# Optimization experiments

Measured on AMD Instinct MI355X. Metric: run time of the kernel, lower is better.

## Reference

```python
import jax, jax.numpy as jnp
import numpy as np

T = 2048          # tokens (single-sequence prefill)
HID = 4096        # hidden_size
NH = 32           # num attention heads
NKV = 8           # num kv heads (GQA)
HD = 128          # head_dim
QKV_OUT = (NH + 2 * NKV) * HD  # 6144
THETA = 10000.0
SCALING = HD ** -0.5


def setup_inputs() -> dict:
    key = jax.random.key(0)
    ks = jax.random.split(key, 8)
    positions = jnp.arange(T, dtype=jnp.int32)
    # per-token int8 quantized hidden states (symmetric, [-127,127])
    q_act = jax.random.randint(ks[0], (T, HID), -127, 128, dtype=jnp.int32)
    # per-token dynamic activation scale
    act_scale = jax.random.uniform(ks[1], (T,), jnp.float32) * 0.01 + 0.001
    # int4 weights stored unsigned [0,15] with per-output-channel scale & zero point
    w_qkv_q = jax.random.randint(ks[2], (QKV_OUT, HID), 0, 16, dtype=jnp.int32)
    w_qkv_scale = jax.random.uniform(ks[3], (QKV_OUT,), jnp.float32) * 0.01 + 0.001
    w_qkv_zero = jax.random.uniform(ks[4], (QKV_OUT,), jnp.float32) * 2.0 + 7.0
    w_o_q = jax.random.randint(ks[5], (HID, HID), 0, 16, dtype=jnp.int32)
    w_o_scale = jax.random.uniform(ks[6], (HID,), jnp.float32) * 0.01 + 0.001
    w_o_zero = jax.random.uniform(ks[7], (HID,), jnp.float32) * 2.0 + 7.0
    return dict(positions=positions, q_act=q_act, act_scale=act_scale,
                w_qkv_q=w_qkv_q, w_qkv_scale=w_qkv_scale, w_qkv_zero=w_qkv_zero,
                w_o_q=w_o_q, w_o_scale=w_o_scale, w_o_zero=w_o_zero)


def w4a8_linear(qa_f, s_a, a_sum, qw, s_w, z_w):
    # y[t,o] = s_a[t]*s_w[o] * ( (qa @ qw^T)[t,o] - z_w[o]*sum_j qa[t,j] )
    acc = jnp.matmul(qa_f, qw.astype(jnp.float32).T)  # [T, O]
    return (s_a[:, None] * s_w[None, :]) * (acc - z_w[None, :] * a_sum[:, None])


def apply_rope(x, positions):
    # neox-style RoPE over full head_dim
    half = HD // 2
    inv_freq = THETA ** (-jnp.arange(0, half, dtype=jnp.float32) / half * 1.0)
    inv_freq = 1.0 / (THETA ** (jnp.arange(0, HD, 2, dtype=jnp.float32) / HD))
    freqs = positions.astype(jnp.float32)[:, None] * inv_freq[None, :]  # [T, HD/2]
    cos = jnp.cos(freqs)[:, None, :]
    sin = jnp.sin(freqs)[:, None, :]
    x1, x2 = x[..., :half], x[..., half:]
    return jnp.concatenate([x1 * cos - x2 * sin, x2 * cos + x1 * sin], axis=-1)


def dynamic_quant_with_sum(x):
    # per-token symmetric int8 dynamic quantization + fused sum
    s = jnp.maximum(jnp.max(jnp.abs(x), axis=-1), 1e-8) / 127.0  # [T]
    q = jnp.clip(jnp.round(x / s[:, None]), -127, 127)
    return q, s, jnp.sum(q, axis=-1)


def reference(positions, q_act, act_scale, w_qkv_q, w_qkv_scale, w_qkv_zero,
              w_o_q, w_o_scale, w_o_zero):
    qa_f = q_act.astype(jnp.float32)
    a_sum = jnp.sum(qa_f, axis=-1)  # fused activation sum
    qkv = w4a8_linear(qa_f, act_scale, a_sum, w_qkv_q, w_qkv_scale, w_qkv_zero)
    q, k, v = jnp.split(qkv, [NH * HD, NH * HD + NKV * HD], axis=-1)
    q = q.reshape(T, NH, HD)
    k = k.reshape(T, NKV, HD)
    v = v.reshape(T, NKV, HD)
    q = apply_rope(q, positions)
    k = apply_rope(k, positions)
    # GQA: repeat kv heads
    rep = NH // NKV
    k = jnp.repeat(k, rep, axis=1)  # [T, NH, HD]
    v = jnp.repeat(v, rep, axis=1)
    scores = jnp.einsum('qhd,khd->hqk', q, k) * SCALING  # [NH, T, T]
    causal = jnp.tril(jnp.ones((T, T), dtype=bool))
    scores = jnp.where(causal[None], scores, -jnp.inf)
    probs = jax.nn.softmax(scores, axis=-1)
    attn = jnp.einsum('hqk,khd->qhd', probs, v).reshape(T, NH * HD)
    # invoke_quant_fuse_sum: dynamic per-token quantization of attn output
    q2, s2, sum2 = dynamic_quant_with_sum(attn)
    out = w4a8_linear(q2, s2, sum2, w_o_q, w_o_scale, w_o_zero)
    return out
```

## Files before the change

kernel.cpp:

```cpp
#include <hip/hip_runtime.h>

#define T 2048
#define HID 4096
#define NH 32
#define NKV 8
#define HD 128
#define QKV_OUT ((NH + 2*NKV) * HD)
#define SCALING 0.08838834764831843f
#define QS2 0.12751744954f
#define DEFER_THR 10.0f
#define ROPE_C 0.20762050593046014f

typedef __attribute__((ext_vector_type(8))) short bfrag;
typedef __attribute__((ext_vector_type(4))) float ffrag;
typedef __attribute__((ext_vector_type(4))) int  ifrag;
typedef __attribute__((ext_vector_type(16))) char c16;

__device__ __forceinline__ short f2bf(float f) {
  unsigned u = __builtin_bit_cast(unsigned, f);
  u += 0x7fffu + ((u >> 16) & 1u);
  return (short)(u >> 16);
}

__device__ __forceinline__ void split2(float x, short& hi, short& lo) {
  unsigned u = __builtin_bit_cast(unsigned, x);
  unsigned uh = u + (0x7fffu + ((u >> 16) & 1u));
  hi = (short)(uh >> 16);
  float fh = __builtin_bit_cast(float, uh & 0xffff0000u);
  float r = x - fh;
  unsigned ur = __builtin_bit_cast(unsigned, r);
  ur += 0x7fffu + ((ur >> 16) & 1u);
  lo = (short)(ur >> 16);
}

__device__ __forceinline__ void gload_lds16(const void* g, void* l) {
  __builtin_amdgcn_global_load_lds(
      (const __attribute__((address_space(1))) unsigned int*)g,
      (__attribute__((address_space(3))) unsigned int*)l, 16, 0, 0);
}


__global__ __launch_bounds__(256)
void prep_a(const int* __restrict__ qact, float* __restrict__ a_sum,
            char* __restrict__ a_i8, float2* __restrict__ tab,
            const int* __restrict__ wsrc, char* __restrict__ wdst) {
  __shared__ int red[256];
  const int bid = blockIdx.x, tid = threadIdx.x;

  if (bid >= T) {
    int idx = (bid - T) * 256 + tid;
    const int4* s4 = (const int4*)wsrc + (size_t)idx * 4;
    c16 o;
#pragma unroll
    for (int j = 0; j < 4; j++) {
      int4 v = s4[j];
      o[j*4+0] = (char)v.x; o[j*4+1] = (char)v.y;
      o[j*4+2] = (char)v.z; o[j*4+3] = (char)v.w;
    }
    const int idxp = (idx & ~7) | ((idx & 7) ^ ((idx >> 8) & 7));
    *(c16*)(wdst + (size_t)idxp * 16) = o;
    return;
  }

  const int t = bid;
  if (t < 512) {
    int idx = t * 256 + tid;
    int p = idx >> 6, j = idx & 63;
    float fr = (float)p * exp2f(-ROPE_C * (float)j);
    float sn, cs; sincosf(fr, &sn, &cs);
    tab[idx] = make_float2(cs, sn);
  }
  const int* row = qact + (size_t)t * HID + tid * 16;
  int s = 0;
  c16 o;
#pragma unroll
  for (int i = 0; i < 4; i++) {
    int4 v = *(const int4*)(row + i * 4);
    s += v.x + v.y + v.z + v.w;
    o[i*4+0] = (char)v.x; o[i*4+1] = (char)v.y;
    o[i*4+2] = (char)v.z; o[i*4+3] = (char)v.w;
  }
  const int chunk = (tid & ~7) | ((tid & 7) ^ (t & 7));
  *(c16*)(a_i8 + (size_t)t * HID + chunk * 16) = o;
  red[tid] = s; __syncthreads();
  for (int off = 128; off > 0; off >>= 1) {
    if (tid < off) red[tid] += red[tid + off];
    __syncthreads();
  }
  if (tid == 0) a_sum[t] = (float)red[0];
}

__global__ __launch_bounds__(256)
void gemm_i8(const char* __restrict__ A, const char* __restrict__ W,
             const float* __restrict__ s_a, const float* __restrict__ asum,
             const float* __restrict__ s_w, const float* __restrict__ z_w,
             float* __restrict__ C, int M, int N, int K) {
  __shared__ __align__(16) char As[2][128 * 128];
  __shared__ __align__(16) char Bs[2][128 * 128];
  const int tid = threadIdx.x;
  const int lane = tid & 63;
  const int quad = lane >> 4, l15 = lane & 15;
  const int wave = tid >> 6;
  const int wm = (wave >> 1) * 64, wn = (wave & 1) * 64;
  const int bm = blockIdx.y * 128, bn = blockIdx.x * 128;
  const int sr = tid >> 3, sc = (tid & 7) * 16;

  ifrag acc[4][4];
#pragma unroll
  for (int mi = 0; mi < 4; mi++)
#pragma unroll
    for (int ni = 0; ni < 4; ni++)
      acc[mi][ni] = (ifrag){0, 0, 0, 0};

  auto stage = [&](int k0, int b) {
#pragma unroll
    for (int j = 0; j < 4; j++) {
      gload_lds16(A + (size_t)(bm + j * 32 + sr) * K + k0 + sc,
                  &As[b][j * 4096 + tid * 16]);
      gload_lds16(W + (size_t)(bn + j * 32 + sr) * K + k0 + sc,
                  &Bs[b][j * 4096 + tid * 16]);
    }
  };

  const int scol0 = ((quad)     ^ (l15 & 7)) * 16;
  const int scol1 = ((4 + quad) ^ (l15 & 7)) * 16;

  stage(0, 0);
  asm volatile("s_waitcnt vmcnt(0)" ::: "memory");
  __builtin_amdgcn_s_barrier();

  int cur = 0;
  for (int k0 = 0; k0 < K; k0 += 128) {
    if (k0 + 128 < K) stage(k0 + 128, cur ^ 1);

#pragma unroll
    for (int ks = 0; ks < 2; ks++) {
      const int scol = ks ? scol1 : scol0;
      ifrag af[4], bfv[4];
#pragma unroll
      for (int mi = 0; mi < 4; mi++)
        af[mi] = *(const ifrag*)&As[cur][(wm + mi * 16 + l15) * 128 + scol];
#pragma unroll
      for (int ni = 0; ni < 4; ni++)
        bfv[ni] = *(const ifrag*)&Bs[cur][(wn + ni * 16 + l15) * 128 + scol];
#pragma unroll
      for (int mi = 0; mi < 4; mi++)
#pragma unroll
        for (int ni = 0; ni < 4; ni++)
          acc[mi][ni] = __builtin_amdgcn_mfma_i32_16x16x64_i8(
              af[mi], bfv[ni], acc[mi][ni], 0, 0, 0);
    }

    asm volatile("s_waitcnt vmcnt(0)" ::: "memory");
    __builtin_amdgcn_s_barrier();
    cur ^= 1;
  }

#pragma unroll
  for (int mi = 0; mi < 4; mi++) {
    int row0 = bm + wm + mi * 16 + quad * 4;
#pragma unroll
    for (int r = 0; r < 4; r++) {
      int row = row0 + r;
      float sa = s_a[row], av = asum[row];
#pragma unroll
      for (int ni = 0; ni < 4; ni++) {
        int col = bn + wn + ni * 16 + l15;
        C[(size_t)row * N + col] = (sa * s_w[col]) * ((float)acc[mi][ni][r] - z_w[col] * av);
      }
    }
  }
}

__global__ __launch_bounds__(256)
void kv_prep(const float* __restrict__ qkv, const int* __restrict__ positions,
             const float2* __restrict__ tab,
             short* __restrict__ Kh, short* __restrict__ Kl,
             short* __restrict__ Vth,
             const int* __restrict__ wsrc, char* __restrict__ wdst) {
  __shared__ __align__(16) short Vh_lds[128 * 72];
  const int bid = blockIdx.x, tid = threadIdx.x;

  if (bid >= 256) {
    int idx = (bid - 256) * 256 + tid;
    const int4* s4 = (const int4*)wsrc + (size_t)idx * 4;
    c16 o;
#pragma unroll
    for (int j = 0; j < 4; j++) {
      int4 v = s4[j];
      o[j*4+0] = (char)v.x; o[j*4+1] = (char)v.y;
      o[j*4+2] = (char)v.z; o[j*4+3] = (char)v.w;
    }
    const int idxp = (idx & ~7) | ((idx & 7) ^ ((idx >> 8) & 7));
    *(c16*)(wdst + (size_t)idxp * 16) = o;
    return;
  }

  const int kvh = bid & 7;
  const int t0 = (bid >> 3) * 64;

#pragma unroll
  for (int it = 0; it < 4; it++) {
    int c = tid + 256 * it;
    int key = c >> 4, dc = c & 15;
    const int t = t0 + key;
    const float* kr = qkv + (size_t)t * QKV_OUT
                      + (size_t)NH * HD + (size_t)kvh * HD;
    float4 a = *(const float4*)(kr + dc * 4);
    float4 b = *(const float4*)(kr + dc * 4 + 64);
    float av[4] = {a.x, a.y, a.z, a.w};
    float bv[4] = {b.x, b.y, b.z, b.w};
    const float2* tr = tab + (size_t)positions[t] * 64 + dc * 4;
    short4 ha, la, hb, lb;
    short hh, ll;
#pragma unroll
    for (int jj = 0; jj < 4; jj++) {
      float cs = tr[jj].x, sn = tr[jj].y;
      float x1 = av[jj], x2 = bv[jj];
      float r1 = x1 * cs - x2 * sn;
      float r2 = x2 * cs + x1 * sn;
      split2(r1, hh, ll); ((short*)&ha)[jj] = hh; ((short*)&la)[jj] = ll;
      split2(r2, hh, ll); ((short*)&hb)[jj] = hh; ((short*)&lb)[jj] = ll;
    }
    const int uu = ((dc >> 1) ^ t) & 7;
    const int h4 = (dc & 1) * 4;
    size_t base = (size_t)kvh * T * HD + (size_t)t * HD;
    *(short4*)(Kh + base + uu * 8 + h4) = ha;
    *(short4*)(Kl + base + uu * 8 + h4) = la;
    *(short4*)(Kh + base + (8 + uu) * 8 + h4) = hb;
    *(short4*)(Kl + base + (8 + uu) * 8 + h4) = lb;
  }
#pragma unroll
  for (int i = 0; i < 8; i++) {
    int c = tid + 256 * i;
    int key = c >> 5, dc = c & 31;
    float4 f = *(const float4*)(qkv + (size_t)(t0 + key) * QKV_OUT
                                + (size_t)(NH + NKV) * HD + (size_t)kvh * HD + dc * 4);
    Vh_lds[(dc*4+0)*72 + key] = f2bf(f.x);
    Vh_lds[(dc*4+1)*72 + key] = f2bf(f.y);
    Vh_lds[(dc*4+2)*72 + key] = f2bf(f.z);
    Vh_lds[(dc*4+3)*72 + key] = f2bf(f.w);
  }
  __syncthreads();
#pragma unroll
  for (int i = 0; i < 2; i++) {
    int c = tid + 256 * i;
    int row = c >> 2, cc = c & 3;
    int sd = (row >> 1) & 3;
    size_t o = (size_t)kvh * HD * T + (size_t)row * T + t0 + ((cc ^ sd)) * 8;
    *(bfrag*)(Vth + o) = *(const bfrag*)&Vh_lds[row * 72 + cc * 8];
  }
#pragma unroll
  for (int i = 0; i < 2; i++) {
    int c = tid + 256 * i;
    int row = c >> 2, cc = c & 3;
    int sd = (row >> 1) & 3;
    size_t o = (size_t)kvh * HD * T + (size_t)row * T + t0 + 32 + ((cc ^ sd)) * 8;
    *(bfrag*)(Vth + o) = *(const bfrag*)&Vh_lds[row * 72 + 32 + cc * 8];
  }
}

__global__ __launch_bounds__(256)
void attn_kernel(const float* __restrict__ qkv, const int* __restrict__ positions,
                 const float2* __restrict__ tab,
                 const short* __restrict__ Kh, const short* __restrict__ Kl,
                 const short* __restrict__ Vth,
                 float* __restrict__ attn) {
  __shared__ __align__(16) short Ksh[2][32 * 128];
  __shared__ __align__(16) short Ksl[2][32 * 128];
  __shared__ __align__(16) short Vsh[2][128 * 32];
  __shared__ __align__(16) short Psh[4 * 16 * 40];

  const int kvh = blockIdx.x & 7;
  const int qt  = 127 - (int)(blockIdx.x >> 3);
  const int tid = threadIdx.x;
  const int lane = tid & 63;
  const int wv = tid >> 6;
  const int l15 = lane & 15, quad = lane >> 4;
  const int h = kvh * 4 + wv;
  short* Pw = Psh + wv * 16 * 40;

  const short* KhB = Kh + (size_t)kvh * T * HD;
  const short* KlB = Kl + (size_t)kvh * T * HD;
  const short* VhB = Vth + (size_t)kvh * HD * T;

  const int offK0 = (tid >> 4) * 128 + (tid & 15) * 8;
  const int offK1 = offK0 + 16 * 128;
  const int offV0 = (tid >> 2) * T + (tid & 3) * 8;
  const int offV1 = offV0 + 64 * T;
  const int wv1k = wv * 1024;

  auto stage = [&](int k0, int b) {
    const short* khs = KhB + (size_t)k0 * HD;
    const short* kls = KlB + (size_t)k0 * HD;
    const short* vs  = VhB + k0;
    gload_lds16(khs + offK0, (char*)&Ksh[b][0] + wv1k);
    gload_lds16(khs + offK1, (char*)&Ksh[b][0] + 4096 + wv1k);
    gload_lds16(kls + offK0, (char*)&Ksl[b][0] + wv1k);
    gload_lds16(kls + offK1, (char*)&Ksl[b][0] + 4096 + wv1k);
    gload_lds16(vs + offV0, (char*)&Vsh[b][0] + wv1k);
    gload_lds16(vs + offV1, (char*)&Vsh[b][0] + 4096 + wv1k);
  };

  const int sdv = (l15 >> 1) & 3;
  const int vq8 = (quad ^ sdv) * 8;
  int uuk[4];
#pragma unroll
  for (int kc = 0; kc < 4; kc++) {
    int s = 4 * kc + quad;
    uuk[kc] = ((s & 8) | ((s ^ l15) & 7)) * 8;
  }

  bfrag ones;
#pragma unroll
  for (int j = 0; j < 8; j++) ones[j] = (short)0x3f80;

  const int q0 = qt * 16;
  const int nk = (q0 >> 5) + 1;

  bfrag qh[4], ql[4];
  {
    const float* qrow = qkv + (size_t)(q0 + l15) * QKV_OUT + (size_t)h * HD;
    float fvv[4][8];
#pragma unroll
    for (int kc = 0; kc < 4; kc++) {
      float4 f0 = *(const float4*)(qrow + kc * 32 + quad * 8);
      float4 f1 = *(const float4*)(qrow + kc * 32 + quad * 8 + 4);
      fvv[kc][0] = f0.x; fvv[kc][1] = f0.y; fvv[kc][2] = f0.z; fvv[kc][3] = f0.w;
      fvv[kc][4] = f1.x; fvv[kc][5] = f1.y; fvv[kc][6] = f1.z; fvv[kc][7] = f1.w;
    }
    const float2* trw = tab + (size_t)positions[q0 + l15] * 64;
#pragma unroll
    for (int kc = 0; kc < 2; kc++) {
#pragma unroll
      for (int j = 0; j < 8; j++) {
        int d = kc * 32 + quad * 8 + j;
        float2 cssn = trw[d];
        float x1 = fvv[kc][j], x2 = fvv[kc + 2][j];
        fvv[kc][j]     = x1 * cssn.x - x2 * cssn.y;
        fvv[kc + 2][j] = x2 * cssn.x + x1 * cssn.y;
      }
    }
#pragma unroll
    for (int kc = 0; kc < 4; kc++)
#pragma unroll
      for (int j = 0; j < 8; j++) {
        short hi, lo; split2(fvv[kc][j] * QS2, hi, lo);
        qh[kc][j] = hi; ql[kc][j] = lo;
      }
  }

  ffrag o[8], ol;
  ol = (ffrag){0.f, 0.f, 0.f, 0.f};
#pragma unroll
  for (int n = 0; n < 8; n++) o[n] = (ffrag){0.f, 0.f, 0.f, 0.f};
  float m_i[4] = {-1e30f, -1e30f, -1e30f, -1e30f};

  auto compute_tile = [&](int k0, int b, bool maskq) {
    const short* ksh = &Ksh[b][0];
    const short* ksl = &Ksl[b][0];
    const short* vsh = &Vsh[b][0];
    ffrag s[2];
    s[0] = (ffrag){0.f,0.f,0.f,0.f}; s[1] = (ffrag){0.f,0.f,0.f,0.f};
#pragma unroll
    for (int kc = 0; kc < 4; kc++) {
#pragma unroll
      for (int n = 0; n < 2; n++) {
        const int rb = (n * 16 + l15) * 128 + uuk[kc];
        bfrag bh = *(const bfrag*)&ksh[rb];
        bfrag bl = *(const bfrag*)&ksl[rb];
        s[n] = __builtin_amdgcn_mfma_f32_16x16x32_bf16(qh[kc], bh, s[n], 0,0,0);
        s[n] = __builtin_amdgcn_mfma_f32_16x16x32_bf16(qh[kc], bl, s[n], 0,0,0);
        s[n] = __builtin_amdgcn_mfma_f32_16x16x32_bf16(ql[kc], bh, s[n], 0,0,0);
      }
    }
    float sv[2][4];
#pragma unroll
    for (int n = 0; n < 2; n++)
#pragma unroll
      for (int r = 0; r < 4; r++) {
        float v = s[n][r];
        if (maskq) {
          int key = k0 + n * 16 + l15;
          int row = q0 + quad * 4 + r;
          if (key > row) v = -1e30f;
        }
        sv[n][r] = v;
      }
    float lm[4];
    bool trig = false;
#pragma unroll
    for (int r = 0; r < 4; r++) {
      lm[r] = fmaxf(sv[0][r], sv[1][r]);
      trig = trig || (lm[r] > m_i[r] + DEFER_THR);
    }
    if (__any(trig)) {
#pragma unroll
      for (int r = 0; r < 4; r++) {
        float m2 = lm[r];
        m2 = fmaxf(m2, __shfl_xor(m2, 1));
        m2 = fmaxf(m2, __shfl_xor(m2, 2));
        m2 = fmaxf(m2, __shfl_xor(m2, 4));
        m2 = fmaxf(m2, __shfl_xor(m2, 8));
        float mn = fmaxf(m_i[r], m2);
        float a = exp2f(m_i[r] - mn);
        m_i[r] = mn;
        ol[r] *= a;
#pragma unroll
        for (int n = 0; n < 8; n++) o[n][r] *= a;
      }
    }
#pragma unroll
    for (int n = 0; n < 2; n++)
#pragma unroll
      for (int r = 0; r < 4; r++) {
        float p = exp2f(sv[n][r] - m_i[r]);
        Pw[(quad*4 + r) * 40 + n*16 + l15] = f2bf(p);
      }
    bfrag ph = *(const bfrag*)&Pw[l15 * 40 + quad * 8];
    ol = __builtin_amdgcn_mfma_f32_16x16x32_bf16(ph, ones, ol, 0,0,0);
#pragma unroll
    for (int n = 0; n < 8; n++) {
      bfrag vh = *(const bfrag*)&vsh[(n * 16 + l15) * 32 + vq8];
      o[n] = __builtin_amdgcn_mfma_f32_16x16x32_bf16(ph, vh, o[n], 0,0,0);
    }
  };

  stage(0, 0);
  asm volatile("s_waitcnt vmcnt(0)" ::: "memory");
  __builtin_amdgcn_s_barrier();

  int cur = 0;
  for (int kt = 0; kt < nk - 1; kt++) {
    const int k0 = kt << 5;
    stage(k0 + 32, cur ^ 1);
    compute_tile(k0, cur, false);
    asm volatile("s_waitcnt vmcnt(0)" ::: "memory");
    __builtin_amdgcn_s_barrier();
    cur ^= 1;
  }
  compute_tile((nk - 1) << 5, cur, true);

  float inv[4];
#pragma unroll
  for (int r = 0; r < 4; r++) inv[r] = 1.f / ol[r];
#pragma unroll
  for (int n = 0; n < 8; n++)
#pragma unroll
    for (int r = 0; r < 4; r++) {
      int row = q0 + quad * 4 + r;
      attn[(size_t)row * HID + (size_t)h * HD + n * 16 + l15] = o[n][r] * inv[r];
    }
}

__global__ __launch_bounds__(256)
void quant_kernel(const float* __restrict__ x, char* __restrict__ q2,
                  float* __restrict__ s2, float* __restrict__ sum2) {
  __shared__ float red[256];
  const int t = blockIdx.x, tid = threadIdx.x;
  const float* row = x + (size_t)t * HID;
  float4 v[4];
  float m = 0.f;
#pragma unroll
  for (int i = 0; i < 4; i++) {
    v[i] = *(const float4*)(row + tid * 16 + i * 4);
    m = fmaxf(m, fmaxf(fmaxf(fabsf(v[i].x), fabsf(v[i].y)),
                       fmaxf(fabsf(v[i].z), fabsf(v[i].w))));
  }
  red[tid] = m; __syncthreads();
  for (int off = 128; off > 0; off >>= 1) {
    if (tid < off) red[tid] = fmaxf(red[tid], red[tid + off]);
    __syncthreads();
  }
  float s = fmaxf(red[0], 1e-8f) / 127.f;
  __syncthreads();
  float ssum = 0.f;
  c16 o;
#pragma unroll
  for (int i = 0; i < 4; i++) {
    float q;
    q = fminf(127.f, fmaxf(-127.f, rintf(v[i].x / s))); ssum += q; o[i*4+0] = (char)(int)q;
    q = fminf(127.f, fmaxf(-127.f, rintf(v[i].y / s))); ssum += q; o[i*4+1] = (char)(int)q;
    q = fminf(127.f, fmaxf(-127.f, rintf(v[i].z / s))); ssum += q; o[i*4+2] = (char)(int)q;
    q = fminf(127.f, fmaxf(-127.f, rintf(v[i].w / s))); ssum += q; o[i*4+3] = (char)(int)q;
  }
  const int chunk = (tid & ~7) | ((tid & 7) ^ (t & 7));
  *(c16*)(q2 + (size_t)t * HID + chunk * 16) = o;
  red[tid] = ssum; __syncthreads();
  for (int off = 128; off > 0; off >>= 1) {
    if (tid < off) red[tid] += red[tid + off];
    __syncthreads();
  }
  if (tid == 0) { s2[t] = s; sum2[t] = red[0]; }
}

extern "C" void kernel_launch(void* const* d_in, const int* in_sizes, int n_in,
                              void* d_out, int out_size, void* d_ws, size_t ws_size,
                              hipStream_t stream) {
  const int*   positions   = (const int*)d_in[0];
  const int*   q_act       = (const int*)d_in[1];
  const float* act_scale   = (const float*)d_in[2];
  const int*   w_qkv_q     = (const int*)d_in[3];
  const float* w_qkv_scale = (const float*)d_in[4];
  const float* w_qkv_zero  = (const float*)d_in[5];
  const int*   w_o_q       = (const int*)d_in[6];
  const float* w_o_scale   = (const float*)d_in[7];
  const float* w_o_zero    = (const float*)d_in[8];
  float* out = (float*)d_out;

  size_t off = 0;
  auto alloc = [&](size_t bytes) -> void* {
    void* p = (char*)d_ws + off;
    off += (bytes + 255) & ~(size_t)255;
    return p;
  };
  float* qkv   = (float*)alloc((size_t)T * QKV_OUT * 4);
  char*  act8  = (char*)alloc((size_t)T * HID);
  char*  w8    = (char*)alloc((size_t)QKV_OUT * HID);
  short* Kh    = (short*)alloc((size_t)NKV * T * HD * 2);
  short* Kl    = (short*)alloc((size_t)NKV * T * HD * 2);
  short* Vth   = (short*)alloc((size_t)NKV * T * HD * 2);
  float* a_sum = (float*)alloc(T * 4);
  float* s2    = (float*)alloc(T * 4);
  float* sum2  = (float*)alloc(T * 4);
  float2* tab  = (float2*)alloc((size_t)T * 64 * 8);
  (void)ws_size;

  prep_a<<<T + QKV_OUT * HID / 16 / 256, 256, 0, stream>>>(
      q_act, a_sum, act8, tab, w_qkv_q, w8);
  gemm_i8<<<dim3(QKV_OUT / 128, T / 128), 256, 0, stream>>>(
      act8, w8, act_scale, a_sum, w_qkv_scale, w_qkv_zero, qkv, T, QKV_OUT, HID);
  kv_prep<<<256 + HID * HID / 16 / 256, 256, 0, stream>>>(
      qkv, positions, tab, Kh, Kl, Vth, w_o_q, w8);
  attn_kernel<<<dim3(1024), 256, 0, stream>>>(
      qkv, positions, tab, Kh, Kl, Vth, out);
  quant_kernel<<<T, 256, 0, stream>>>(out, act8, s2, sum2);
  gemm_i8<<<dim3(HID / 128, T / 128), 256, 0, stream>>>(
      act8, w8, s2, sum2, w_o_scale, w_o_zero, out, T, HID, HID);
}
```

Baseline: 463.7 us.

## Process two 16-row query tiles per attention block to reuse K/V loads

Each attention block now handles 32 query rows (two 16-row groups) per KV head instead of 16, so every staged K/V tile in LDS feeds twice as many MFMAs, and the grid is halved to 512 blocks. Block ordering is remapped so the heaviest causal tiles are scheduled first. The change cuts global and LDS traffic per unit of work, at the cost of more registers per wave, possibly lower occupancy, and fewer blocks to spread across the CUs.

```diff
diff --git a/kernel.cpp b/kernel.cpp
--- a/kernel.cpp
+++ b/kernel.cpp
@@ -269,16 +269,20 @@
   __shared__ __align__(16) short Ksh[2][32 * 128];
   __shared__ __align__(16) short Ksl[2][32 * 128];
   __shared__ __align__(16) short Vsh[2][128 * 32];
-  __shared__ __align__(16) short Psh[4 * 16 * 40];
+  __shared__ __align__(16) short Psh[4 * 2 * 16 * 40];
 
   const int kvh = blockIdx.x & 7;
-  const int qt  = 127 - (int)(blockIdx.x >> 3);
+  const int i6 = blockIdx.x >> 3;
+  const int g  = (i6 < 32) ? (63 - i6) : (i6 - 32);
+  const int nk = g + 1;
+  const int q00 = g * 32, q01 = g * 32 + 16;
   const int tid = threadIdx.x;
   const int lane = tid & 63;
   const int wv = tid >> 6;
   const int l15 = lane & 15, quad = lane >> 4;
   const int h = kvh * 4 + wv;
-  short* Pw = Psh + wv * 16 * 40;
+  short* Pw0 = Psh + wv * 1280;
+  short* Pw1 = Pw0 + 640;
 
   const short* KhB = Kh + (size_t)kvh * T * HD;
   const short* KlB = Kl + (size_t)kvh * T * HD;
@@ -315,11 +319,10 @@
 #pragma unroll
   for (int j = 0; j < 8; j++) ones[j] = (short)0x3f80;
 
-  const int q0 = qt * 16;
-  const int nk = (q0 >> 5) + 1;
-
-  bfrag qh[4], ql[4];
-  {
+  bfrag qh0[4], ql0[4], qh1[4], ql1[4];
+#pragma unroll
+  for (int rg = 0; rg < 2; rg++) {
+    const int q0 = rg ? q01 : q00;
     const float* qrow = qkv + (size_t)(q0 + l15) * QKV_OUT + (size_t)h * HD;
     float fvv[4][8];
 #pragma unroll
@@ -346,22 +349,29 @@
 #pragma unroll
       for (int j = 0; j < 8; j++) {
         short hi, lo; split2(fvv[kc][j] * QS2, hi, lo);
-        qh[kc][j] = hi; ql[kc][j] = lo;
-      }
-  }
-
-  ffrag o[8], ol;
-  ol = (ffrag){0.f, 0.f, 0.f, 0.f};
-#pragma unroll
-  for (int n = 0; n < 8; n++) o[n] = (ffrag){0.f, 0.f, 0.f, 0.f};
-  float m_i[4] = {-1e30f, -1e30f, -1e30f, -1e30f};
+        if (rg) { qh1[kc][j] = hi; ql1[kc][j] = lo; }
+        else    { qh0[kc][j] = hi; ql0[kc][j] = lo; }
+      }
+  }
+
+  ffrag o0[8], o1[8], ol0, ol1;
+  ol0 = (ffrag){0.f, 0.f, 0.f, 0.f};
+  ol1 = (ffrag){0.f, 0.f, 0.f, 0.f};
+#pragma unroll
+  for (int n = 0; n < 8; n++) {
+    o0[n] = (ffrag){0.f, 0.f, 0.f, 0.f};
+    o1[n] = (ffrag){0.f, 0.f, 0.f, 0.f};
+  }
+  float m0[4] = {-1e30f, -1e30f, -1e30f, -1e30f};
+  float m1[4] = {-1e30f, -1e30f, -1e30f, -1e30f};
 
   auto compute_tile = [&](int k0, int b, bool maskq) {
     const short* ksh = &Ksh[b][0];
     const short* ksl = &Ksl[b][0];
     const short* vsh = &Vsh[b][0];
-    ffrag s[2];
-    s[0] = (ffrag){0.f,0.f,0.f,0.f}; s[1] = (ffrag){0.f,0.f,0.f,0.f};
+    ffrag s0[2], s1[2];
+    s0[0] = (ffrag){0.f,0.f,0.f,0.f}; s0[1] = (ffrag){0.f,0.f,0.f,0.f};
+    s1[0] = (ffrag){0.f,0.f,0.f,0.f}; s1[1] = (ffrag){0.f,0.f,0.f,0.f};
 #pragma unroll
     for (int kc = 0; kc < 4; kc++) {
 #pragma unroll
@@ -369,60 +379,77 @@
         const int rb = (n * 16 + l15) * 128 + uuk[kc];
         bfrag bh = *(const bfrag*)&ksh[rb];
         bfrag bl = *(const bfrag*)&ksl[rb];
-        s[n] = __builtin_amdgcn_mfma_f32_16x16x32_bf16(qh[kc], bh, s[n], 0,0,0);
-        s[n] = __builtin_amdgcn_mfma_f32_16x16x32_bf16(qh[kc], bl, s[n], 0,0,0);
-        s[n] = __builtin_amdgcn_mfma_f32_16x16x32_bf16(ql[kc], bh, s[n], 0,0,0);
-      }
-    }
-    float sv[2][4];
+        s0[n] = __builtin_amdgcn_mfma_f32_16x16x32_bf16(qh0[kc], bh, s0[n], 0,0,0);
+        s0[n] = __builtin_amdgcn_mfma_f32_16x16x32_bf16(qh0[kc], bl, s0[n], 0,0,0);
+        s0[n] = __builtin_amdgcn_mfma_f32_16x16x32_bf16(ql0[kc], bh, s0[n], 0,0,0);
+        s1[n] = __builtin_amdgcn_mfma_f32_16x16x32_bf16(qh1[kc], bh, s1[n], 0,0,0);
+        s1[n] = __builtin_amdgcn_mfma_f32_16x16x32_bf16(qh1[kc], bl, s1[n], 0,0,0);
+        s1[n] = __builtin_amdgcn_mfma_f32_16x16x32_bf16(ql1[kc], bh, s1[n], 0,0,0);
+      }
+    }
+    float sv0[2][4], sv1[2][4], lm0[4], lm1[4];
+    bool trig = false;
 #pragma unroll
     for (int n = 0; n < 2; n++)
 #pragma unroll
       for (int r = 0; r < 4; r++) {
-        float v = s[n][r];
+        float v0 = s0[n][r], v1 = s1[n][r];
         if (maskq) {
           int key = k0 + n * 16 + l15;
-          int row = q0 + quad * 4 + r;
-          if (key > row) v = -1e30f;
+          int row0r = q00 + quad * 4 + r;
+          int row1r = q01 + quad * 4 + r;
+          if (key > row0r) v0 = -1e30f;
+          if (key > row1r) v1 = -1e30f;
         }
-        sv[n][r] = v;
-      }
-    float lm[4];
-    bool trig = false;
+        sv0[n][r] = v0; sv1[n][r] = v1;
+      }
 #pragma unroll
     for (int r = 0; r < 4; r++) {
-      lm[r] = fmaxf(sv[0][r], sv[1][r]);
-      trig = trig || (lm[r] > m_i[r] + DEFER_THR);
+      lm0[r] = fmaxf(sv0[0][r], sv0[1][r]);
+      lm1[r] = fmaxf(sv1[0][r], sv1[1][r]);
+      trig = trig || (lm0[r] > m0[r] + DEFER_THR) || (lm1[r] > m1[r] + DEFER_THR);
     }
     if (__any(trig)) {
 #pragma unroll
       for (int r = 0; r < 4; r++) {
-        float m2 = lm[r];
-        m2 = fmaxf(m2, __shfl_xor(m2, 1));
-        m2 = fmaxf(m2, __shfl_xor(m2, 2));
-        m2 = fmaxf(m2, __shfl_xor(m2, 4));
-        m2 = fmaxf(m2, __shfl_xor(m2, 8));
-        float mn = fmaxf(m_i[r], m2);
-        float a = exp2f(m_i[r] - mn);
-        m_i[r] = mn;
-        ol[r] *= a;
-#pragma unroll
-        for (int n = 0; n < 8; n++) o[n][r] *= a;
+        float a2 = lm0[r];
+        a2 = fmaxf(a2, __shfl_xor(a2, 1));
+        a2 = fmaxf(a2, __shfl_xor(a2, 2));
+        a2 = fmaxf(a2, __shfl_xor(a2, 4));
+        a2 = fmaxf(a2, __shfl_xor(a2, 8));
+        float mn = fmaxf(m0[r], a2);
+        float a = exp2f(m0[r] - mn);
+        m0[r] = mn; ol0[r] *= a;
+#pragma unroll
+        for (int n = 0; n < 8; n++) o0[n][r] *= a;
+        float b2 = lm1[r];
+        b2 = fmaxf(b2, __shfl_xor(b2, 1));
+        b2 = fmaxf(b2, __shfl_xor(b2, 2));
+        b2 = fmaxf(b2, __shfl_xor(b2, 4));
+        b2 = fmaxf(b2, __shfl_xor(b2, 8));
+        float mn1 = fmaxf(m1[r], b2);
+        float a1 = exp2f(m1[r] - mn1);
+        m1[r] = mn1; ol1[r] *= a1;
+#pragma unroll
+        for (int n = 0; n < 8; n++) o1[n][r] *= a1;
       }
     }
 #pragma unroll
     for (int n = 0; n < 2; n++)
 #pragma unroll
       for (int r = 0; r < 4; r++) {
-        float p = exp2f(sv[n][r] - m_i[r]);
-        Pw[(quad*4 + r) * 40 + n*16 + l15] = f2bf(p);
-      }
-    bfrag ph = *(const bfrag*)&Pw[l15 * 40 + quad * 8];
-    ol = __builtin_amdgcn_mfma_f32_16x16x32_bf16(ph, ones, ol, 0,0,0);
+        Pw0[(quad*4 + r) * 40 + n*16 + l15] = f2bf(exp2f(sv0[n][r] - m0[r]));
+        Pw1[(quad*4 + r) * 40 + n*16 + l15] = f2bf(exp2f(sv1[n][r] - m1[r]));
+      }
+    bfrag ph0 = *(const bfrag*)&Pw0[l15 * 40 + quad * 8];
+    bfrag ph1 = *(const bfrag*)&Pw1[l15 * 40 + quad * 8];
+    ol0 = __builtin_amdgcn_mfma_f32_16x16x32_bf16(ph0, ones, ol0, 0,0,0);
+    ol1 = __builtin_amdgcn_mfma_f32_16x16x32_bf16(ph1, ones, ol1, 0,0,0);
 #pragma unroll
     for (int n = 0; n < 8; n++) {
       bfrag vh = *(const bfrag*)&vsh[(n * 16 + l15) * 32 + vq8];
-      o[n] = __builtin_amdgcn_mfma_f32_16x16x32_bf16(ph, vh, o[n], 0,0,0);
+      o0[n] = __builtin_amdgcn_mfma_f32_16x16x32_bf16(ph0, vh, o0[n], 0,0,0);
+      o1[n] = __builtin_amdgcn_mfma_f32_16x16x32_bf16(ph1, vh, o1[n], 0,0,0);
     }
   };
 
@@ -441,15 +468,17 @@
   }
   compute_tile((nk - 1) << 5, cur, true);
 
-  float inv[4];
-#pragma unroll
-  for (int r = 0; r < 4; r++) inv[r] = 1.f / ol[r];
+  float inv0[4], inv1[4];
+#pragma unroll
+  for (int r = 0; r < 4; r++) { inv0[r] = 1.f / ol0[r]; inv1[r] = 1.f / ol1[r]; }
 #pragma unroll
   for (int n = 0; n < 8; n++)
 #pragma unroll
     for (int r = 0; r < 4; r++) {
-      int row = q0 + quad * 4 + r;
-      attn[(size_t)row * HID + (size_t)h * HD + n * 16 + l15] = o[n][r] * inv[r];
+      int row0r = q00 + quad * 4 + r;
+      int row1r = q01 + quad * 4 + r;
+      attn[(size_t)row0r * HID + (size_t)h * HD + n * 16 + l15] = o0[n][r] * inv0[r];
+      attn[(size_t)row1r * HID + (size_t)h * HD + n * 16 + l15] = o1[n][r] * inv1[r];
     }
 }
 
@@ -532,7 +561,7 @@
       act8, w8, act_scale, a_sum, w_qkv_scale, w_qkv_zero, qkv, T, QKV_OUT, HID);
   kv_prep<<<256 + HID * HID / 16 / 256, 256, 0, stream>>>(
       qkv, positions, tab, Kh, Kl, Vth, w_o_q, w8);
-  attn_kernel<<<dim3(1024), 256, 0, stream>>>(
+  attn_kernel<<<dim3(512), 256, 0, stream>>>(
       qkv, positions, tab, Kh, Kl, Vth, out);
   quant_kernel<<<T, 256, 0, stream>>>(out, act8, s2, sum2);
   gemm_i8<<<dim3(HID / 128, T / 128), 256, 0, stream>>>(
```

After: 526.2 us. 13.5% more time.
